# Kernel optimization log

Hardware: AMD Instinct MI355X
Metric: run time of the kernel (lower is better)

Reference implementation:

```python
import jax, jax.numpy as jnp
import numpy as np

H, DK, NF, DC, B, T = 8, 64, 512, 256, 8, 1024

def setup_inputs() -> dict:
    key = jax.random.key(0)
    ks = jax.random.split(key, 16)
    s = lambda fan_in: 1.0 / np.sqrt(fan_in)
    return {
        "x": jax.random.normal(ks[0], (B, T, NF), jnp.float32),
        "cond": jax.random.normal(ks[1], (B, T, DC), jnp.float32),
        "pos_k": jax.random.normal(ks[2], (T, T, DK), jnp.float32),
        "mask": jax.random.randint(ks[3], (B, T, T), 0, 2, jnp.int32),
        "ln_gamma": jnp.ones((NF,), jnp.float32),
        "ln_beta": jnp.zeros((NF,), jnp.float32),
        "Wq": jax.random.uniform(ks[4], (NF, NF), jnp.float32, -s(NF), s(NF)),
        "bq": jax.random.uniform(ks[5], (NF,), jnp.float32, -s(NF), s(NF)),
        "Wk": jax.random.uniform(ks[6], (NF, NF), jnp.float32, -s(NF), s(NF)),
        "bk": jax.random.uniform(ks[7], (NF,), jnp.float32, -s(NF), s(NF)),
        "Wv": jax.random.uniform(ks[8], (NF, NF), jnp.float32, -s(NF), s(NF)),
        "bv": jax.random.uniform(ks[9], (NF,), jnp.float32, -s(NF), s(NF)),
        "Wo": jax.random.uniform(ks[10], (NF, NF), jnp.float32, -s(NF), s(NF)),
        "bo": jax.random.uniform(ks[11], (NF,), jnp.float32, -s(NF), s(NF)),
        "Wc": jax.random.uniform(ks[12], (DC, NF), jnp.float32, -s(DC), s(DC)),
        "bc": jax.random.uniform(ks[13], (NF,), jnp.float32, -s(DC), s(DC)),
    }

def reference(x, cond, pos_k, mask, ln_gamma, ln_beta, Wq, bq, Wk, bk, Wv, bv, Wo, bo, Wc, bc):
    # LayerNorm over features (eps matches torch default)
    mu = jnp.mean(x, axis=-1, keepdims=True)
    var = jnp.mean(jnp.square(x - mu), axis=-1, keepdims=True)
    xn = (x - mu) * jax.lax.rsqrt(var + 1e-5) * ln_gamma + ln_beta
    # projections; query comes from conditioning signal
    q = ((cond @ Wc + bc) @ Wq + bq).reshape(B, T, H, DK)
    k = (xn @ Wk + bk).reshape(B, T, H, DK)
    v = (xn @ Wv + bv).reshape(B, T, H, DK)
    # content scores + relative-position bias (matmul-trick equivalent)
    A = jnp.einsum('bthd,bshd->bhts', q, k)
    Bbias = jnp.einsum('bthd,tsd->bhts', q, pos_k)
    scores = (A + Bbias) / np.sqrt(DK)
    m0 = (mask == 0)[:, None, :, :]  # (B,1,T,T) True where masked
    min_val = jnp.finfo(scores.dtype).min
    scores = jnp.where(m0, min_val, scores)
    attn = jnp.where(m0, 0.0, jax.nn.softmax(scores, axis=-1))
    out = jnp.einsum('bhts,bshd->bthd', attn, v).reshape(B, T, NF)
    return out @ Wo + bo
```

## Files before the change

kernel.cpp:

```cpp
#include <hip/hip_runtime.h>

#define Bb 8
#define Tt 1024
#define Hh 8
#define DKk 64
#define NFf 512
#define DCc 256

typedef _Float16 v2h __attribute__((ext_vector_type(2)));
typedef _Float16 v4h __attribute__((ext_vector_type(4)));
typedef _Float16 v8h __attribute__((ext_vector_type(8)));
typedef float    v4f __attribute__((ext_vector_type(4)));
typedef float    v16f __attribute__((ext_vector_type(16)));

#define MFMA32(a,b,c) __builtin_amdgcn_mfma_f32_16x16x32_f16((a),(b),(c),0,0,0)
#define MFMA3216(a,b,c) __builtin_amdgcn_mfma_f32_32x32x16_f16((a),(b),(c),0,0,0)

#define SCQ 0.1803368801111f

__device__ inline void st8(_Float16* dst, v8h x){
    *(v4h*)dst     = __builtin_shufflevector(x,x,0,1,2,3);
    *(v4h*)(dst+4) = __builtin_shufflevector(x,x,4,5,6,7);
}

__device__ inline v8h cvt8(float4 a, float4 b){
    v8h r;
    r[0]=(_Float16)a.x; r[1]=(_Float16)a.y; r[2]=(_Float16)a.z; r[3]=(_Float16)a.w;
    r[4]=(_Float16)b.x; r[5]=(_Float16)b.y; r[6]=(_Float16)b.z; r[7]=(_Float16)b.w;
    return r;
}

__device__ inline v4f ntl4(const float* p){
    return __builtin_nontemporal_load(reinterpret_cast<const v4f*>(p));
}

__device__ inline int swz(int r, int c){ return (r*64 + c) ^ ((r&7)<<3); }

__global__ __launch_bounds__(256) void k_front(const float* __restrict__ x,
                                               const float* __restrict__ g,
                                               const float* __restrict__ be,
                                               _Float16* __restrict__ xn,
                                               const float* __restrict__ Wk,
                                               const float* __restrict__ Wv,
                                               const float* __restrict__ Wo,
                                               const float* __restrict__ Wq,
                                               _Float16* __restrict__ WkT,
                                               _Float16* __restrict__ WvT,
                                               _Float16* __restrict__ WoT,
                                               _Float16* __restrict__ WqT,
                                               const float* __restrict__ Wc,
                                               _Float16* __restrict__ WcH,
                                               const float* __restrict__ bq,
                                               float* __restrict__ bcq,
                                               float* __restrict__ zero){
    __shared__ float smem[64*65];
    int bid = blockIdx.x;
    int tid = threadIdx.x;
    if (bid < 320){
        int z = bid >> 6;
        int xy = bid & 63;
        if (z < 4){
            const float* W = (z==0)?Wk:(z==1)?Wv:(z==2)?Wo:Wq;
            _Float16*  WT = (z==0)?WkT:(z==1)?WvT:(z==2)?WoT:WqT;
            int bx = (xy&7)*64, by = (xy>>3)*64;
            int c = tid&63;
            float (*tile)[65] = (float(*)[65])smem;
            for (int r = tid>>6; r<64; r+=4) tile[r][c] = W[(size_t)(by+r)*512 + bx + c];
            __syncthreads();
            for (int n = tid>>6; n<64; n+=4) WT[(size_t)(bx+n)*512 + by + c] = (_Float16)tile[c][n];
        } else {
            int i = (xy*256 + tid)*8;
            float4 a = *(const float4*)(Wc+i);
            float4 b2 = *(const float4*)(Wc+i+4);
            *(v8h*)(WcH+i) = cvt8(a,b2);
            if (xy == 0) zero[tid] = 0.f;
            if (xy == 1){ bcq[tid] = bq[tid]; bcq[tid+256] = bq[tid+256]; }
        }
        return;
    }
    int row = bid - 320;
    const float* xr = x + (size_t)row*512;
    float2 v = reinterpret_cast<const float2*>(xr)[tid];
    float s = v.x + v.y, sq = v.x*v.x + v.y*v.y;
    for (int off=32; off; off>>=1){ s += __shfl_down(s, off); sq += __shfl_down(sq, off); }
    int wid = tid>>6, lid = tid&63;
    if (lid==0){ smem[wid]=s; smem[4+wid]=sq; }
    __syncthreads();
    if (tid==0){
        float S=0,Q=0;
        for(int i=0;i<4;i++){S+=smem[i];Q+=smem[4+i];}
        float mu = S*(1.f/512.f);
        float var = Q*(1.f/512.f)-mu*mu;
        smem[8]=mu; smem[9]=rsqrtf(var+1e-5f);
    }
    __syncthreads();
    float mu=smem[8], rs=smem[9];
    float2 gv = reinterpret_cast<const float2*>(g)[tid];
    float2 bv = reinterpret_cast<const float2*>(be)[tid];
    v2h o; o[0] = (_Float16)((v.x-mu)*rs*gv.x + bv.x);
           o[1] = (_Float16)((v.y-mu)*rs*gv.y + bv.y);
    reinterpret_cast<v2h*>(xn + (size_t)row*512)[tid] = o;
}

__global__ __launch_bounds__(512) void k_bcqp(const float* __restrict__ bc,
                                              const float* __restrict__ Wq,
                                              float* __restrict__ bcq){
    int j = threadIdx.x; int m0 = blockIdx.x*16;
    float a = 0.f;
    #pragma unroll
    for (int m=0;m<16;m++) a += bc[m0+m]*Wq[(size_t)(m0+m)*512 + j];
    atomicAdd(&bcq[j], a);
}

template<typename AT, typename CT>
__global__ __launch_bounds__(512) void k_gemm(const AT* __restrict__ A,
                                              const _Float16* __restrict__ WT,
                                              const float* __restrict__ bias,
                                              CT* __restrict__ C,
                                              int M, int N, int K,
                                              float scale){
    __shared__ _Float16 Al[2][128*64];
    __shared__ _Float16 Wl[2][128*64];
    int tid = threadIdx.x, l = tid&63, w = tid>>6;
    int l15 = l&15, lq = l>>4;
    int wr = w>>2, wc = w&3;
    int m0 = blockIdx.y*128, n0 = blockIdx.x*128;
    v4f acc[4][2] = {};
    float bv[2];
    #pragma unroll
    for (int bc=0;bc<2;++bc) bv[bc] = bias[n0 + wc*32 + bc*16 + l15];
    int srow = tid>>2, sseg = (tid&3)*16;
    const AT* arow = A + (size_t)(m0+srow)*K + sseg;
    const _Float16* wrow = WT + (size_t)(n0+srow)*K + sseg;
    int NT = K>>6;

    v8h pa0, pa1, pw0, pw1;
    if constexpr (sizeof(AT)==4){
        const float* s = (const float*)arow;
        pa0 = cvt8(*(const float4*)s,     *(const float4*)(s+4));
        pa1 = cvt8(*(const float4*)(s+8), *(const float4*)(s+12));
    } else {
        pa0 = *(const v8h*)arow; pa1 = *(const v8h*)(arow+8);
    }
    pw0 = *(const v8h*)wrow; pw1 = *(const v8h*)(wrow+8);
    st8(&Al[0][swz(srow,sseg)], pa0); st8(&Al[0][swz(srow,sseg+8)], pa1);
    st8(&Wl[0][swz(srow,sseg)], pw0); st8(&Wl[0][swz(srow,sseg+8)], pw1);
    __syncthreads();

    for (int kt=0; kt<NT; ++kt){
        int cur = kt&1;
        if (kt < NT-1){
            int k0 = (kt+1)<<6;
            if constexpr (sizeof(AT)==4){
                const float* s = (const float*)arow + k0;
                pa0 = cvt8(*(const float4*)s,     *(const float4*)(s+4));
                pa1 = cvt8(*(const float4*)(s+8), *(const float4*)(s+12));
            } else {
                pa0 = *(const v8h*)(arow + k0); pa1 = *(const v8h*)(arow + k0 + 8);
            }
            pw0 = *(const v8h*)(wrow + k0); pw1 = *(const v8h*)(wrow + k0 + 8);
        }
        #pragma unroll
        for (int kk=0; kk<2; ++kk){
            v8h af[4], bf[2];
            #pragma unroll
            for (int ar=0;ar<4;++ar) af[ar] = *(v8h*)&Al[cur][swz(wr*64+ar*16+l15, kk*32+lq*8)];
            #pragma unroll
            for (int bc=0;bc<2;++bc) bf[bc] = *(v8h*)&Wl[cur][swz(wc*32+bc*16+l15, kk*32+lq*8)];
            #pragma unroll
            for (int ar=0;ar<4;++ar)
                #pragma unroll
                for (int bc=0;bc<2;++bc)
                    acc[ar][bc] = MFMA32(af[ar], bf[bc], acc[ar][bc]);
        }
        if (kt < NT-1){
            st8(&Al[cur^1][swz(srow,sseg)], pa0); st8(&Al[cur^1][swz(srow,sseg+8)], pa1);
            st8(&Wl[cur^1][swz(srow,sseg)], pw0); st8(&Wl[cur^1][swz(srow,sseg+8)], pw1);
        }
        __syncthreads();
    }
    #pragma unroll
    for (int ar=0;ar<4;++ar){
        #pragma unroll
        for (int bc=0;bc<2;++bc){
            #pragma unroll
            for (int i=0;i<4;++i){
                int row = m0 + wr*64 + ar*16 + lq*4 + i;
                int col = n0 + wc*32 + bc*16 + l15;
                float vf = (acc[ar][bc][i] + bv[bc])*scale;
                C[(size_t)row*N + col] = (CT)vf;
            }
        }
    }
}

__global__ __launch_bounds__(512) void k_gemmkv(const _Float16* __restrict__ A,
                                                const _Float16* __restrict__ WTk,
                                                const _Float16* __restrict__ WTv,
                                                const float* __restrict__ bk,
                                                const float* __restrict__ bv,
                                                _Float16* __restrict__ Ck,
                                                _Float16* __restrict__ Cv){
    __shared__ _Float16 Al[2][128*64];
    __shared__ _Float16 Wkl[2][128*64];
    __shared__ _Float16 Wvl[2][128*64];
    int tid = threadIdx.x, l = tid&63, w = tid>>6;
    int l15 = l&15, lq = l>>4;
    int wr = w>>2, wc = w&3;
    int m0 = blockIdx.y*128, n0 = blockIdx.x*128;
    v4f ack[4][2] = {}, acv[4][2] = {};
    float bkr[2], bvr[2];
    #pragma unroll
    for (int bc=0;bc<2;++bc){ bkr[bc] = bk[n0 + wc*32 + bc*16 + l15]; bvr[bc] = bv[n0 + wc*32 + bc*16 + l15]; }
    int srow = tid>>2, sseg = (tid&3)*16;
    const _Float16* arow = A   + (size_t)(m0+srow)*512 + sseg;
    const _Float16* krow = WTk + (size_t)(n0+srow)*512 + sseg;
    const _Float16* vrow = WTv + (size_t)(n0+srow)*512 + sseg;

    v8h pa0,pa1,pk0,pk1,pv0,pv1;
    pa0 = *(const v8h*)arow; pa1 = *(const v8h*)(arow+8);
    pk0 = *(const v8h*)krow; pk1 = *(const v8h*)(krow+8);
    pv0 = *(const v8h*)vrow; pv1 = *(const v8h*)(vrow+8);
    st8(&Al[0][swz(srow,sseg)],  pa0); st8(&Al[0][swz(srow,sseg+8)],  pa1);
    st8(&Wkl[0][swz(srow,sseg)], pk0); st8(&Wkl[0][swz(srow,sseg+8)], pk1);
    st8(&Wvl[0][swz(srow,sseg)], pv0); st8(&Wvl[0][swz(srow,sseg+8)], pv1);
    __syncthreads();

    for (int kt=0; kt<8; ++kt){
        int cur = kt&1;
        if (kt < 7){
            int k0 = (kt+1)<<6;
            pa0 = *(const v8h*)(arow+k0); pa1 = *(const v8h*)(arow+k0+8);
            pk0 = *(const v8h*)(krow+k0); pk1 = *(const v8h*)(krow+k0+8);
            pv0 = *(const v8h*)(vrow+k0); pv1 = *(const v8h*)(vrow+k0+8);
        }
        #pragma unroll
        for (int kk=0; kk<2; ++kk){
            v8h af[4], kf[2], vf[2];
            #pragma unroll
            for (int ar=0;ar<4;++ar) af[ar] = *(v8h*)&Al[cur][swz(wr*64+ar*16+l15, kk*32+lq*8)];
            #pragma unroll
            for (int bc=0;bc<2;++bc){
                kf[bc] = *(v8h*)&Wkl[cur][swz(wc*32+bc*16+l15, kk*32+lq*8)];
                vf[bc] = *(v8h*)&Wvl[cur][swz(wc*32+bc*16+l15, kk*32+lq*8)];
            }
            #pragma unroll
            for (int ar=0;ar<4;++ar)
                #pragma unroll
                for (int bc=0;bc<2;++bc){
                    ack[ar][bc] = MFMA32(af[ar], kf[bc], ack[ar][bc]);
                    acv[ar][bc] = MFMA32(af[ar], vf[bc], acv[ar][bc]);
                }
        }
        if (kt < 7){
            st8(&Al[cur^1][swz(srow,sseg)],  pa0); st8(&Al[cur^1][swz(srow,sseg+8)],  pa1);
            st8(&Wkl[cur^1][swz(srow,sseg)], pk0); st8(&Wkl[cur^1][swz(srow,sseg+8)], pk1);
            st8(&Wvl[cur^1][swz(srow,sseg)], pv0); st8(&Wvl[cur^1][swz(srow,sseg+8)], pv1);
        }
        __syncthreads();
    }
    #pragma unroll
    for (int ar=0;ar<4;++ar){
        #pragma unroll
        for (int bc=0;bc<2;++bc){
            #pragma unroll
            for (int i=0;i<4;++i){
                int row = m0 + wr*64 + ar*16 + lq*4 + i;
                int col = n0 + wc*32 + bc*16 + l15;
                Ck[(size_t)row*512 + col] = (_Float16)(ack[ar][bc][i] + bkr[bc]);
                Cv[(size_t)row*512 + col] = (_Float16)(acv[ar][bc][i] + bvr[bc]);
            }
        }
    }
}

__global__ __launch_bounds__(256) void k_bias(const _Float16* __restrict__ qbuf,
                                              const float* __restrict__ posk,
                                              const int* __restrict__ mask,
                                              _Float16* __restrict__ Sb){
    __shared__ _Float16 Pl[64*64];
    __shared__ _Float16 Ol[64*72];
    int t = blockIdx.x >> 1, sh = blockIdx.x & 1;
    int tid = threadIdx.x, l = tid&63, w = tid>>6;
    int l31 = l&31, hi = l>>5;
    int g = w & 1, sg = w >> 1;
    v8h aa[4];
    {
        int bh = g*32 + l31; int bI = bh>>3, hI = bh&7;
        const _Float16* qrow = qbuf + ((size_t)(bI*Tt + t))*NFf + hI*DKk + hi*8;
        #pragma unroll
        for (int k0=0;k0<4;++k0)
            aa[k0] = *(const v8h*)(qrow + k0*16);
    }

    const float* pkt = posk + ((size_t)t<<16);
    int sbase = sh*512;
    int lrow = (l>>4), lcol = (l&15)*4;

    v4f pf[4];
    #pragma unroll
    for (int j=0;j<4;++j)
        pf[j] = ntl4(pkt + (size_t)(sbase + w*16 + j*4 + lrow)*64 + lcol);

    int obh = tid>>2;
    int osl = (tid&3)*16;
    int ob  = obh>>3;
    const int* mbase = mask + (((size_t)(ob*Tt + t))<<10);
    _Float16* sbb = Sb + (((size_t)(t*64 + obh))<<10);

    #pragma unroll
    for (int j=0;j<4;++j){
        v4h hv; hv[0]=(_Float16)pf[j][0]; hv[1]=(_Float16)pf[j][1];
                hv[2]=(_Float16)pf[j][2]; hv[3]=(_Float16)pf[j][3];
        *(v4h*)&Pl[swz(w*16 + j*4 + lrow, lcol)] = hv;
    }
    __syncthreads();

    for (int sc=0; sc<8; ++sc){
        int s0 = sbase + sc*64;
        if (sc < 7){
            #pragma unroll
            for (int j=0;j<4;++j)
                pf[j] = ntl4(pkt + (size_t)(s0 + 64 + w*16 + j*4 + lrow)*64 + lcol);
        }
        int4 mq[4];
        #pragma unroll
        for (int j=0;j<4;++j)
            mq[j] = *(const int4*)(mbase + s0 + osl + j*4);
        v8h bfr[4];
        #pragma unroll
        for (int k0=0;k0<4;++k0)
            bfr[k0] = *(v8h*)&Pl[swz(sg*32 + l31, k0*16 + hi*8)];
        v16f acc = {};
        #pragma unroll
        for (int k0=0;k0<4;++k0) acc = MFMA3216(aa[k0], bfr[k0], acc);
        #pragma unroll
        for (int r=0;r<16;++r){
            int bh = g*32 + (r&3) + 4*hi + 8*(r>>2);
            Ol[bh*72 + sg*32 + l31] = (_Float16)acc[r];
        }
        __syncthreads();
        if (sc < 7){
            #pragma unroll
            for (int j=0;j<4;++j){
                v4h hv; hv[0]=(_Float16)pf[j][0]; hv[1]=(_Float16)pf[j][1];
                        hv[2]=(_Float16)pf[j][2]; hv[3]=(_Float16)pf[j][3];
                *(v4h*)&Pl[swz(w*16 + j*4 + lrow, lcol)] = hv;
            }
        }
        v8h o0 = *(v8h*)&Ol[obh*72 + osl];
        v8h o1 = *(v8h*)&Ol[obh*72 + osl + 8];
        const _Float16 NEG = (_Float16)(-30000.f);
        int mm[16] = {mq[0].x,mq[0].y,mq[0].z,mq[0].w, mq[1].x,mq[1].y,mq[1].z,mq[1].w,
                      mq[2].x,mq[2].y,mq[2].z,mq[2].w, mq[3].x,mq[3].y,mq[3].z,mq[3].w};
        #pragma unroll
        for (int j=0;j<8;++j){ if(!mm[j]) o0[j]=NEG; if(!mm[8+j]) o1[j]=NEG; }
        *(v8h*)(sbb + s0 + osl)     = o0;
        *(v8h*)(sbb + s0 + osl + 8) = o1;
        __syncthreads();
    }
}

__global__ __launch_bounds__(512) void k_flash(const _Float16* __restrict__ qs,
                                               const _Float16* __restrict__ kbuf,
                                               const _Float16* __restrict__ vbuf,
                                               const _Float16* __restrict__ Sb,
                                               _Float16* __restrict__ ao){
    __shared__ _Float16 Kl[2][64*64];
    __shared__ _Float16 Vt[2][64*64];
    __shared__ _Float16 Bl[2][128*64];
    int bh = blockIdx.x; int b = bh>>3, h = bh&7;
    int t0 = blockIdx.y*128;
    int tid = threadIdx.x, l = tid&63, w = tid>>6, l15 = l&15, lq = l>>4;

    v8h qa[2];
    #pragma unroll
    for (int u=0;u<2;++u)
        qa[u] = *(const v8h*)(qs + ((size_t)(b*Tt + t0 + w*16 + l15))*NFf + h*DKk + u*32 + lq*8);

    v4f O[4] = {};
    float m_l = -1e30f, l_l = 0.f;

    int kr = tid>>3, kseg = (tid&7)*8;
    int vs = tid&63, vd0 = (tid>>6)*8;
    int br = tid>>2, bhf = (tid&3)*16;
    const _Float16* kbase = kbuf + ((size_t)(b*Tt + kr))*NFf + h*DKk + kseg;
    const _Float16* vbase = vbuf + ((size_t)(b*Tt + vs))*NFf + h*DKk + vd0;
    const _Float16* bbase = Sb + (((size_t)((t0+br)*64 + bh))<<10) + bhf;

    v8h pk = *(const v8h*)kbase;
    v8h pv = *(const v8h*)vbase;
    v8h pb0 = *(const v8h*)bbase;
    v8h pb1 = *((const v8h*)bbase + 1);
    st8(&Kl[0][swz(kr, kseg)], pk);
    #pragma unroll
    for (int j=0;j<8;j++) Vt[0][swz(vd0+j, vs)] = pv[j];
    st8(&Bl[0][swz(br, bhf)],   pb0);
    st8(&Bl[0][swz(br, bhf+8)], pb1);
    __syncthreads();

    for (int sc=0; sc<16; ++sc){
        int cur = sc&1;
        if (sc < 15){
            size_t soff = (size_t)(sc+1)*64;
            pk  = *(const v8h*)(kbase + soff*NFf);
            pv  = *(const v8h*)(vbase + soff*NFf);
            pb0 = *(const v8h*)(bbase + soff);
            pb1 = *((const v8h*)(bbase + soff) + 1);
        }

        v4f sv[4];
        #pragma unroll
        for (int nt=0; nt<4; ++nt){
            v8h kb0 = *(v8h*)&Kl[cur][swz(nt*16+l15, lq*8)];
            v8h kb1 = *(v8h*)&Kl[cur][swz(nt*16+l15, 32+lq*8)];
            v4f a = {};
            a = MFMA32(kb0, qa[0], a);
            a = MFMA32(kb1, qa[1], a);
            v4h bl4 = *(v4h*)&Bl[cur][swz(w*16 + l15, nt*16 + lq*4)];
            #pragma unroll
            for (int i=0;i<4;i++) a[i] += (float)bl4[i];
            sv[nt] = a;
        }
        float mx = fmaxf(fmaxf(fmaxf(sv[0][0],sv[0][1]),fmaxf(sv[0][2],sv[0][3])),
                   fmaxf(fmaxf(fmaxf(sv[1][0],sv[1][1]),fmaxf(sv[1][2],sv[1][3])),
                   fmaxf(fmaxf(fmaxf(sv[2][0],sv[2][1]),fmaxf(sv[2][2],sv[2][3])),
                         fmaxf(fmaxf(sv[3][0],sv[3][1]),fmaxf(sv[3][2],sv[3][3])))));
        mx = fmaxf(mx, __shfl_xor(mx,16));
        mx = fmaxf(mx, __shfl_xor(mx,32));
        float mn = fmaxf(m_l, mx);
        if (__any(mn - m_l > 0.f)){
            float rsc = exp2f(m_l - mn);
            m_l = mn; l_l *= rsc;
            float rscB[4];
            #pragma unroll
            for (int i=0;i<4;i++) rscB[i] = __shfl(rsc, lq*4+i);
            #pragma unroll
            for (int nt=0; nt<4; ++nt)
                #pragma unroll
                for (int i=0;i<4;i++) O[nt][i] *= rscB[i];
        }
        float ps = 0.f;
        #pragma unroll
        for (int nt=0; nt<4; ++nt){
            v4h ph;
            #pragma unroll
            for (int i=0;i<4;i++){
                float p = exp2f(sv[nt][i] - m_l);
                ph[i] = (_Float16)p;
                ps += p;
            }
            *(v4h*)&Bl[cur][swz(w*16 + l15, nt*16 + lq*4)] = ph;
        }
        ps += __shfl_xor(ps,16);
        ps += __shfl_xor(ps,32);
        l_l += ps;
        {
            v8h pa0 = *(v8h*)&Bl[cur][swz(w*16+l15, lq*8)];
            v8h pa1 = *(v8h*)&Bl[cur][swz(w*16+l15, 32+lq*8)];
            #pragma unroll
            for (int nt=0; nt<4; ++nt){
                v8h vb0 = *(v8h*)&Vt[cur][swz(nt*16+l15, lq*8)];
                v8h vb1 = *(v8h*)&Vt[cur][swz(nt*16+l15, 32+lq*8)];
                O[nt] = MFMA32(pa0, vb0, O[nt]);
                O[nt] = MFMA32(pa1, vb1, O[nt]);
            }
        }
        if (sc < 15){
            st8(&Kl[cur^1][swz(kr, kseg)], pk);
            #pragma unroll
            for (int j=0;j<8;j++) Vt[cur^1][swz(vd0+j, vs)] = pv[j];
            st8(&Bl[cur^1][swz(br, bhf)],   pb0);
            st8(&Bl[cur^1][swz(br, bhf+8)], pb1);
        }
        __syncthreads();
    }

    float rl = (l_l > 0.f) ? 1.f/l_l : 0.f;
    float rlB[4];
    #pragma unroll
    for (int i=0;i<4;i++) rlB[i] = __shfl(rl, lq*4+i);
    #pragma unroll
    for (int i=0;i<4;i++){
        int row = t0 + w*16 + lq*4 + i;
        #pragma unroll
        for (int nt=0; nt<4; ++nt)
            ao[((size_t)(b*Tt + row))*NFf + h*DKk + nt*16 + l15] = (_Float16)(O[nt][i]*rlB[i]);
    }
}

extern "C" void kernel_launch(void* const* d_in, const int* in_sizes, int n_in,
                              void* d_out, int out_size, void* d_ws, size_t ws_size,
                              hipStream_t stream) {
    const float* x       = (const float*)d_in[0];
    const float* cond    = (const float*)d_in[1];
    const float* pos_k   = (const float*)d_in[2];
    const int*   mask    = (const int*)  d_in[3];
    const float* ln_g    = (const float*)d_in[4];
    const float* ln_b    = (const float*)d_in[5];
    const float* Wq      = (const float*)d_in[6];
    const float* bq      = (const float*)d_in[7];
    const float* Wk      = (const float*)d_in[8];
    const float* bk      = (const float*)d_in[9];
    const float* Wv      = (const float*)d_in[10];
    const float* bv      = (const float*)d_in[11];
    const float* Wo      = (const float*)d_in[12];
    const float* bo      = (const float*)d_in[13];
    const float* Wc      = (const float*)d_in[14];
    const float* bc      = (const float*)d_in[15];
    float* out = (float*)d_out;

    char* base = (char*)d_ws;
    const size_t OFF_S    = 0;
    const size_t OFF_XN   = 134217728;
    const size_t OFF_Q    = OFF_XN  + 8388608;
    const size_t OFF_K    = OFF_Q   + 8388608;
    const size_t OFF_V    = OFF_K   + 8388608;
    const size_t OFF_AO   = OFF_V   + 8388608;
    const size_t OFF_WKT  = OFF_AO  + 8388608;
    const size_t OFF_WVT  = OFF_WKT + 524288;
    const size_t OFF_WOT  = OFF_WVT + 524288;
    const size_t OFF_WQT  = OFF_WOT + 524288;
    const size_t OFF_WCH  = OFF_WQT + 524288;
    const size_t OFF_WCQT = OFF_WCH + 262144;
    const size_t OFF_BCQ  = OFF_WCQT + 262144;
    const size_t OFF_ZERO = OFF_BCQ + 2048;

    _Float16* xn    = (_Float16*)(base + OFF_XN);
    _Float16* qbuf  = (_Float16*)(base + OFF_Q);
    _Float16* kb    = (_Float16*)(base + OFF_K);
    _Float16* vb    = (_Float16*)(base + OFF_V);
    _Float16* ao    = (_Float16*)(base + OFF_AO);
    _Float16* Sb    = (_Float16*)(base + OFF_S);
    _Float16* WkT   = (_Float16*)(base + OFF_WKT);
    _Float16* WvT   = (_Float16*)(base + OFF_WVT);
    _Float16* WoT   = (_Float16*)(base + OFF_WOT);
    _Float16* WqT   = (_Float16*)(base + OFF_WQT);
    _Float16* WcH   = (_Float16*)(base + OFF_WCH);
    _Float16* wcqT  = (_Float16*)(base + OFF_WCQT);
    float*    bcq   = (float*)(base + OFF_BCQ);
    float*    zero  = (float*)(base + OFF_ZERO);

    k_front<<<dim3(8512), dim3(256), 0, stream>>>(x, ln_g, ln_b, xn,
                                                  Wk, Wv, Wo, Wq, WkT, WvT, WoT, WqT,
                                                  Wc, WcH, bq, bcq, zero);
    k_bcqp<<<dim3(16), dim3(512), 0, stream>>>(bc, Wq, bcq);

    k_gemm<_Float16,_Float16><<<dim3(2,4), dim3(512), 0, stream>>>(WqT, WcH, zero, wcqT, 512, 256, 512, 1.f);

    k_gemm<float,_Float16><<<dim3(4,64), dim3(512), 0, stream>>>(cond, wcqT, bcq, qbuf, Bb*Tt, 512, 256, SCQ);
    k_gemmkv<<<dim3(4,64), dim3(512), 0, stream>>>(xn, WkT, WvT, bk, bv, kb, vb);

    k_bias<<<dim3(2048), dim3(256), 0, stream>>>(qbuf, pos_k, mask, Sb);
    k_flash<<<dim3(64,8), dim3(512), 0, stream>>>(qbuf, kb, vb, Sb, ao);

    k_gemm<_Float16,float><<<dim3(4,64), dim3(512), 0, stream>>>(ao, WoT, bo, out, Bb*Tt, 512, 512, 1.f);
}
```

Before: 185.2 us.

## Merge Q and KV projections into one launch, single-buffer flash bias tile

The Q projection (cond × fused Wc·Wq) and the K/V projection GEMMs now run as one kernel. The grid's z index selects the path, so both projections fill the device together and one launch is saved. k_bias gets a launch-bounds occupancy hint, and its mask loads move after the barrier to shorten register live ranges. k_flash drops the double buffer for the bias/P tile in LDS, which cuts shared-memory use but relies on each wave only touching its own rows.

New measurement: 189.1 us. 1.02x slower.

```diff
diff --git a/kernel.cpp b/kernel.cpp
--- a/kernel.cpp
+++ b/kernel.cpp
@@ -194,38 +194,95 @@
     }
 }
 
-__global__ __launch_bounds__(512) void k_gemmkv(const _Float16* __restrict__ A,
-                                                const _Float16* __restrict__ WTk,
-                                                const _Float16* __restrict__ WTv,
-                                                const float* __restrict__ bk,
-                                                const float* __restrict__ bv,
-                                                _Float16* __restrict__ Ck,
-                                                _Float16* __restrict__ Cv){
-    __shared__ _Float16 Al[2][128*64];
-    __shared__ _Float16 Wkl[2][128*64];
-    __shared__ _Float16 Wvl[2][128*64];
+__global__ __launch_bounds__(512) void k_projall(const float* __restrict__ cond,
+                                                 const _Float16* __restrict__ wcqT,
+                                                 const float* __restrict__ bcq,
+                                                 _Float16* __restrict__ qbuf,
+                                                 const _Float16* __restrict__ xn,
+                                                 const _Float16* __restrict__ WTk,
+                                                 const _Float16* __restrict__ WTv,
+                                                 const float* __restrict__ bk,
+                                                 const float* __restrict__ bv,
+                                                 _Float16* __restrict__ Ck,
+                                                 _Float16* __restrict__ Cv){
+    __shared__ _Float16 S1[2][128*64];
+    __shared__ _Float16 S2[2][128*64];
+    __shared__ _Float16 S3[2][128*64];
     int tid = threadIdx.x, l = tid&63, w = tid>>6;
     int l15 = l&15, lq = l>>4;
     int wr = w>>2, wc = w&3;
     int m0 = blockIdx.y*128, n0 = blockIdx.x*128;
+    int srow = tid>>2, sseg = (tid&3)*16;
+
+    if (blockIdx.z == 0){
+        v4f acc[4][2] = {};
+        float bvr[2];
+        #pragma unroll
+        for (int bc=0;bc<2;++bc) bvr[bc] = bcq[n0 + wc*32 + bc*16 + l15];
+        const float* arow = cond + (size_t)(m0+srow)*256 + sseg;
+        const _Float16* wrow = wcqT + (size_t)(n0+srow)*256 + sseg;
+        v8h pa0, pa1, pw0, pw1;
+        pa0 = cvt8(*(const float4*)arow,     *(const float4*)(arow+4));
+        pa1 = cvt8(*(const float4*)(arow+8), *(const float4*)(arow+12));
+        pw0 = *(const v8h*)wrow; pw1 = *(const v8h*)(wrow+8);
+        st8(&S1[0][swz(srow,sseg)], pa0); st8(&S1[0][swz(srow,sseg+8)], pa1);
+        st8(&S2[0][swz(srow,sseg)], pw0); st8(&S2[0][swz(srow,sseg+8)], pw1);
+        __syncthreads();
+        for (int kt=0; kt<4; ++kt){
+            int cur = kt&1;
+            if (kt < 3){
+                int k0 = (kt+1)<<6;
+                pa0 = cvt8(*(const float4*)(arow+k0),   *(const float4*)(arow+k0+4));
+                pa1 = cvt8(*(const float4*)(arow+k0+8), *(const float4*)(arow+k0+12));
+                pw0 = *(const v8h*)(wrow + k0); pw1 = *(const v8h*)(wrow + k0 + 8);
+            }
+            #pragma unroll
+            for (int kk=0; kk<2; ++kk){
+                v8h af[4], bf[2];
+                #pragma unroll
+                for (int ar=0;ar<4;++ar) af[ar] = *(v8h*)&S1[cur][swz(wr*64+ar*16+l15, kk*32+lq*8)];
+                #pragma unroll
+                for (int bc=0;bc<2;++bc) bf[bc] = *(v8h*)&S2[cur][swz(wc*32+bc*16+l15, kk*32+lq*8)];
+                #pragma unroll
+                for (int ar=0;ar<4;++ar)
+                    #pragma unroll
+                    for (int bc=0;bc<2;++bc)
+                        acc[ar][bc] = MFMA32(af[ar], bf[bc], acc[ar][bc]);
+            }
+            if (kt < 3){
+                st8(&S1[cur^1][swz(srow,sseg)], pa0); st8(&S1[cur^1][swz(srow,sseg+8)], pa1);
+                st8(&S2[cur^1][swz(srow,sseg)], pw0); st8(&S2[cur^1][swz(srow,sseg+8)], pw1);
+            }
+            __syncthreads();
+        }
+        #pragma unroll
+        for (int ar=0;ar<4;++ar)
+            #pragma unroll
+            for (int bc=0;bc<2;++bc)
+                #pragma unroll
+                for (int i=0;i<4;++i){
+                    int row = m0 + wr*64 + ar*16 + lq*4 + i;
+                    int col = n0 + wc*32 + bc*16 + l15;
+                    qbuf[(size_t)row*512 + col] = (_Float16)((acc[ar][bc][i] + bvr[bc])*SCQ);
+                }
+        return;
+    }
+
     v4f ack[4][2] = {}, acv[4][2] = {};
     float bkr[2], bvr[2];
     #pragma unroll
     for (int bc=0;bc<2;++bc){ bkr[bc] = bk[n0 + wc*32 + bc*16 + l15]; bvr[bc] = bv[n0 + wc*32 + bc*16 + l15]; }
-    int srow = tid>>2, sseg = (tid&3)*16;
-    const _Float16* arow = A   + (size_t)(m0+srow)*512 + sseg;
+    const _Float16* arow = xn  + (size_t)(m0+srow)*512 + sseg;
     const _Float16* krow = WTk + (size_t)(n0+srow)*512 + sseg;
     const _Float16* vrow = WTv + (size_t)(n0+srow)*512 + sseg;
-
     v8h pa0,pa1,pk0,pk1,pv0,pv1;
     pa0 = *(const v8h*)arow; pa1 = *(const v8h*)(arow+8);
     pk0 = *(const v8h*)krow; pk1 = *(const v8h*)(krow+8);
     pv0 = *(const v8h*)vrow; pv1 = *(const v8h*)(vrow+8);
-    st8(&Al[0][swz(srow,sseg)],  pa0); st8(&Al[0][swz(srow,sseg+8)],  pa1);
-    st8(&Wkl[0][swz(srow,sseg)], pk0); st8(&Wkl[0][swz(srow,sseg+8)], pk1);
-    st8(&Wvl[0][swz(srow,sseg)], pv0); st8(&Wvl[0][swz(srow,sseg+8)], pv1);
+    st8(&S1[0][swz(srow,sseg)], pa0); st8(&S1[0][swz(srow,sseg+8)], pa1);
+    st8(&S2[0][swz(srow,sseg)], pk0); st8(&S2[0][swz(srow,sseg+8)], pk1);
+    st8(&S3[0][swz(srow,sseg)], pv0); st8(&S3[0][swz(srow,sseg+8)], pv1);
     __syncthreads();
-
     for (int kt=0; kt<8; ++kt){
         int cur = kt&1;
         if (kt < 7){
@@ -238,11 +295,11 @@
         for (int kk=0; kk<2; ++kk){
             v8h af[4], kf[2], vf[2];
             #pragma unroll
-            for (int ar=0;ar<4;++ar) af[ar] = *(v8h*)&Al[cur][swz(wr*64+ar*16+l15, kk*32+lq*8)];
+            for (int ar=0;ar<4;++ar) af[ar] = *(v8h*)&S1[cur][swz(wr*64+ar*16+l15, kk*32+lq*8)];
             #pragma unroll
             for (int bc=0;bc<2;++bc){
-                kf[bc] = *(v8h*)&Wkl[cur][swz(wc*32+bc*16+l15, kk*32+lq*8)];
-                vf[bc] = *(v8h*)&Wvl[cur][swz(wc*32+bc*16+l15, kk*32+lq*8)];
+                kf[bc] = *(v8h*)&S2[cur][swz(wc*32+bc*16+l15, kk*32+lq*8)];
+                vf[bc] = *(v8h*)&S3[cur][swz(wc*32+bc*16+l15, kk*32+lq*8)];
             }
             #pragma unroll
             for (int ar=0;ar<4;++ar)
@@ -253,16 +310,16 @@
                 }
         }
         if (kt < 7){
-            st8(&Al[cur^1][swz(srow,sseg)],  pa0); st8(&Al[cur^1][swz(srow,sseg+8)],  pa1);
-            st8(&Wkl[cur^1][swz(srow,sseg)], pk0); st8(&Wkl[cur^1][swz(srow,sseg+8)], pk1);
-            st8(&Wvl[cur^1][swz(srow,sseg)], pv0); st8(&Wvl[cur^1][swz(srow,sseg+8)], pv1);
+            st8(&S1[cur^1][swz(srow,sseg)], pa0); st8(&S1[cur^1][swz(srow,sseg+8)], pa1);
+            st8(&S2[cur^1][swz(srow,sseg)], pk0); st8(&S2[cur^1][swz(srow,sseg+8)], pk1);
+            st8(&S3[cur^1][swz(srow,sseg)], pv0); st8(&S3[cur^1][swz(srow,sseg+8)], pv1);
         }
         __syncthreads();
     }
     #pragma unroll
-    for (int ar=0;ar<4;++ar){
-        #pragma unroll
-        for (int bc=0;bc<2;++bc){
+    for (int ar=0;ar<4;++ar)
+        #pragma unroll
+        for (int bc=0;bc<2;++bc)
             #pragma unroll
             for (int i=0;i<4;++i){
                 int row = m0 + wr*64 + ar*16 + lq*4 + i;
@@ -270,14 +327,12 @@
                 Ck[(size_t)row*512 + col] = (_Float16)(ack[ar][bc][i] + bkr[bc]);
                 Cv[(size_t)row*512 + col] = (_Float16)(acv[ar][bc][i] + bvr[bc]);
             }
-        }
-    }
-}
-
-__global__ __launch_bounds__(256) void k_bias(const _Float16* __restrict__ qbuf,
-                                              const float* __restrict__ posk,
-                                              const int* __restrict__ mask,
-                                              _Float16* __restrict__ Sb){
+}
+
+__global__ __launch_bounds__(256,6) void k_bias(const _Float16* __restrict__ qbuf,
+                                                const float* __restrict__ posk,
+                                                const int* __restrict__ mask,
+                                                _Float16* __restrict__ Sb){
     __shared__ _Float16 Pl[64*64];
     __shared__ _Float16 Ol[64*72];
     int t = blockIdx.x >> 1, sh = blockIdx.x & 1;
@@ -323,10 +378,6 @@
             for (int j=0;j<4;++j)
                 pf[j] = ntl4(pkt + (size_t)(s0 + 64 + w*16 + j*4 + lrow)*64 + lcol);
         }
-        int4 mq[4];
-        #pragma unroll
-        for (int j=0;j<4;++j)
-            mq[j] = *(const int4*)(mbase + s0 + osl + j*4);
         v8h bfr[4];
         #pragma unroll
         for (int k0=0;k0<4;++k0)
@@ -340,6 +391,10 @@
             Ol[bh*72 + sg*32 + l31] = (_Float16)acc[r];
         }
         __syncthreads();
+        int4 mq[4];
+        #pragma unroll
+        for (int j=0;j<4;++j)
+            mq[j] = *(const int4*)(mbase + s0 + osl + j*4);
         if (sc < 7){
             #pragma unroll
             for (int j=0;j<4;++j){
@@ -368,7 +423,7 @@
                                                _Float16* __restrict__ ao){
     __shared__ _Float16 Kl[2][64*64];
     __shared__ _Float16 Vt[2][64*64];
-    __shared__ _Float16 Bl[2][128*64];
+    __shared__ _Float16 Bl[128*64];
     int bh = blockIdx.x; int b = bh>>3, h = bh&7;
     int t0 = blockIdx.y*128;
     int tid = threadIdx.x, l = tid&63, w = tid>>6, l15 = l&15, lq = l>>4;
@@ -395,8 +450,8 @@
     st8(&Kl[0][swz(kr, kseg)], pk);
     #pragma unroll
     for (int j=0;j<8;j++) Vt[0][swz(vd0+j, vs)] = pv[j];
-    st8(&Bl[0][swz(br, bhf)],   pb0);
-    st8(&Bl[0][swz(br, bhf+8)], pb1);
+    st8(&Bl[swz(br, bhf)],   pb0);
+    st8(&Bl[swz(br, bhf+8)], pb1);
     __syncthreads();
 
     for (int sc=0; sc<16; ++sc){
@@ -417,7 +472,7 @@
             v4f a = {};
             a = MFMA32(kb0, qa[0], a);
             a = MFMA32(kb1, qa[1], a);
-            v4h bl4 = *(v4h*)&Bl[cur][swz(w*16 + l15, nt*16 + lq*4)];
+            v4h bl4 = *(v4h*)&Bl[swz(w*16 + l15, nt*16 + lq*4)];
             #pragma unroll
             for (int i=0;i<4;i++) a[i] += (float)bl4[i];
             sv[nt] = a;
@@ -450,14 +505,14 @@
                 ph[i] = (_Float16)p;
                 ps += p;
             }
-            *(v4h*)&Bl[cur][swz(w*16 + l15, nt*16 + lq*4)] = ph;
+            *(v4h*)&Bl[swz(w*16 + l15, nt*16 + lq*4)] = ph;
         }
         ps += __shfl_xor(ps,16);
         ps += __shfl_xor(ps,32);
         l_l += ps;
         {
-            v8h pa0 = *(v8h*)&Bl[cur][swz(w*16+l15, lq*8)];
-            v8h pa1 = *(v8h*)&Bl[cur][swz(w*16+l15, 32+lq*8)];
+            v8h pa0 = *(v8h*)&Bl[swz(w*16+l15, lq*8)];
+            v8h pa1 = *(v8h*)&Bl[swz(w*16+l15, 32+lq*8)];
             #pragma unroll
             for (int nt=0; nt<4; ++nt){
                 v8h vb0 = *(v8h*)&Vt[cur][swz(nt*16+l15, lq*8)];
@@ -470,8 +525,8 @@
             st8(&Kl[cur^1][swz(kr, kseg)], pk);
             #pragma unroll
             for (int j=0;j<8;j++) Vt[cur^1][swz(vd0+j, vs)] = pv[j];
-            st8(&Bl[cur^1][swz(br, bhf)],   pb0);
-            st8(&Bl[cur^1][swz(br, bhf+8)], pb1);
+            st8(&Bl[swz(br, bhf)],   pb0);
+            st8(&Bl[swz(br, bhf+8)], pb1);
         }
         __syncthreads();
     }
@@ -548,8 +603,8 @@
 
     k_gemm<_Float16,_Float16><<<dim3(2,4), dim3(512), 0, stream>>>(WqT, WcH, zero, wcqT, 512, 256, 512, 1.f);
 
-    k_gemm<float,_Float16><<<dim3(4,64), dim3(512), 0, stream>>>(cond, wcqT, bcq, qbuf, Bb*Tt, 512, 256, SCQ);
-    k_gemmkv<<<dim3(4,64), dim3(512), 0, stream>>>(xn, WkT, WvT, bk, bv, kb, vb);
+    k_projall<<<dim3(4,64,2), dim3(512), 0, stream>>>(cond, wcqT, bcq, qbuf,
+                                                      xn, WkT, WvT, bk, bv, kb, vb);
 
     k_bias<<<dim3(2048), dim3(256), 0, stream>>>(qbuf, pos_k, mask, Sb);
     k_flash<<<dim3(64,8), dim3(512), 0, stream>>>(qbuf, kb, vb, Sb, ao);
```
